# Kernel optimization log

Measured on AMD Instinct MI355X. Metric: run time of the kernel, lower is better.

The kernel has to match this reference:

```python
import jax, jax.numpy as jnp
import numpy as np

CELLS = 56
EPS = 1e-9

def setup_inputs() -> dict:
    key = jax.random.key(0)
    k1, k2 = jax.random.split(key)
    B = 512
    F = CELLS * CELLS * 15  # 47040 floats per sample
    output = jax.random.uniform(k1, (B, F), dtype=jnp.float32)
    target = jax.random.uniform(k2, (B, F), dtype=jnp.float32)
    return {"output": output, "target": target}

def reference(output, target):
    B = output.shape[0]
    # reshape flat vector into [B, cells^2, 15] slots: x,y,w,h,conf,classes[5:14]
    o = output.reshape(B, CELLS * CELLS, 15)
    t = target.reshape(B, CELLS * CELLS, 15)
    # coordinate loss: only x (slice [i*15 : i*15+1]) plus sqrt(w)/sqrt(h) terms
    coord = (o[..., 0] - t[..., 0]) ** 2 \
          + (jnp.sqrt(o[..., 2]) - jnp.sqrt(t[..., 2])) ** 2 \
          + (jnp.sqrt(o[..., 3]) - jnp.sqrt(t[..., 3])) ** 2
    # binary cross-entropy on confidence (slot 4)
    conf = -(t[..., 4] * jnp.log(o[..., 4] + EPS)
             + (1.0 - t[..., 4]) * jnp.log(1.0 - o[..., 4] + EPS))
    # class loss: sum of squared diffs over slots 5:14 (9 elements)
    cls = jnp.sum((t[..., 5:14] - o[..., 5:14]) ** 2, axis=-1)
    # cell is counted only if output x-coordinate is nonzero (torch.is_nonzero gate)
    mask = o[..., 0] != 0
    per_cell = jnp.where(mask, coord + conf + cls, 0.0)
    return jnp.sum(per_cell)
```

## Files before the change

### kernel.cpp

```cpp
#include <hip/hip_runtime.h>


constexpr int CPT = 256;
constexpr int TF  = CPT * 15;
#define EPSF 1e-9f

__global__ __launch_bounds__(256) void yolo_loss_kernel(
    const float* __restrict__ o, const float* __restrict__ t,
    float* __restrict__ out_sum, int n_cells)
{
    __shared__ __align__(16) float so[TF];
    __shared__ __align__(16) float st[TF];
    __shared__ float wsum[4];

    const int tid = threadIdx.x;
    const int n_tiles = (n_cells + CPT - 1) / CPT;
    const long lim4 = ((long)n_cells * 15) / 4;
    const float4* o4 = (const float4*)o;
    const float4* t4 = (const float4*)t;

    float acc = 0.f;

    for (int tile = blockIdx.x; tile < n_tiles; tile += gridDim.x) {
        __syncthreads();
        const long b4 = (long)tile * (TF / 4);
        #pragma unroll
        for (int i = tid; i < TF / 4; i += 256) {
            long g = b4 + i;
            if (g < lim4) {
                ((float4*)so)[i] = o4[g];
                ((float4*)st)[i] = t4[g];
            }
        }
        __syncthreads();

        const int cell = tile * CPT + tid;
        if (cell < n_cells) {
            const float* oc = so + tid * 15;
            const float* tc = st + tid * 15;
            const float o0 = oc[0];
            if (o0 != 0.f) {
                const float d0 = o0 - tc[0];
                const float dw = sqrtf(oc[2]) - sqrtf(tc[2]);
                const float dh = sqrtf(oc[3]) - sqrtf(tc[3]);
                const float tv = tc[4], ov = oc[4];
                const float conf = -(tv * __logf(ov + EPSF)
                                   + (1.f - tv) * __logf(1.f - ov + EPSF));
                float s = d0 * d0 + dw * dw + dh * dh + conf;
                #pragma unroll
                for (int k = 5; k < 14; ++k) {
                    const float d = tc[k] - oc[k];
                    s += d * d;
                }
                acc += s;
            }
        }
    }

    #pragma unroll
    for (int off = 32; off; off >>= 1) acc += __shfl_down(acc, off, 64);
    if ((tid & 63) == 0) wsum[tid >> 6] = acc;
    __syncthreads();
    if (tid == 0) atomicAdd(out_sum, wsum[0] + wsum[1] + wsum[2] + wsum[3]);
}

extern "C" void kernel_launch(void* const* d_in, const int* in_sizes, int n_in,
                              void* d_out, int out_size, void* d_ws, size_t ws_size,
                              hipStream_t stream) {
    const float* o = (const float*)d_in[0];
    const float* t = (const float*)d_in[1];
    float* out = (float*)d_out;
    const int n = in_sizes[0];
    const int n_cells = n / 15;

    hipMemsetAsync(out, 0, sizeof(float), stream);

    const int grid = 1024;
    yolo_loss_kernel<<<grid, 256, 0, stream>>>(o, t, out, n_cells);
}
```

Measured before the change: 207.4 us.

## Load four-cell groups directly into registers instead of staging through LDS

```diff
diff --git a/kernel.cpp b/kernel.cpp
--- a/kernel.cpp
+++ b/kernel.cpp
@@ -1,64 +1,79 @@
 #include <hip/hip_runtime.h>
 
 
-constexpr int CPT = 256;
-constexpr int TF  = CPT * 15;
 #define EPSF 1e-9f
 
 __global__ __launch_bounds__(256) void yolo_loss_kernel(
     const float* __restrict__ o, const float* __restrict__ t,
     float* __restrict__ out_sum, int n_cells)
 {
-    __shared__ __align__(16) float so[TF];
-    __shared__ __align__(16) float st[TF];
-    __shared__ float wsum[4];
-
     const int tid = threadIdx.x;
-    const int n_tiles = (n_cells + CPT - 1) / CPT;
-    const long lim4 = ((long)n_cells * 15) / 4;
-    const float4* o4 = (const float4*)o;
-    const float4* t4 = (const float4*)t;
+    const int g   = blockIdx.x * 256 + tid;
+    const int n_groups = n_cells >> 2;
 
     float acc = 0.f;
 
-    for (int tile = blockIdx.x; tile < n_tiles; tile += gridDim.x) {
-        __syncthreads();
-        const long b4 = (long)tile * (TF / 4);
+    if (g < n_groups) {
+        const float4* o4 = (const float4*)o + (size_t)g * 15;
+        const float4* t4 = (const float4*)t + (size_t)g * 15;
+
+        float4 ob[15], tb[15];
         #pragma unroll
-        for (int i = tid; i < TF / 4; i += 256) {
-            long g = b4 + i;
-            if (g < lim4) {
-                ((float4*)so)[i] = o4[g];
-                ((float4*)st)[i] = t4[g];
+        for (int j = 0; j < 15; ++j) { ob[j] = o4[j]; tb[j] = t4[j]; }
+        const float* os = (const float*)ob;
+        const float* ts = (const float*)tb;
+
+        float csum[4], x0[4];
+        #pragma unroll
+        for (int c = 0; c < 4; ++c) {
+            const float* oc = os + c * 15;
+            const float* tc = ts + c * 15;
+            x0[c] = oc[0];
+            const float d0 = oc[0] - tc[0];
+            const float dw = sqrtf(oc[2]) - sqrtf(tc[2]);
+            const float dh = sqrtf(oc[3]) - sqrtf(tc[3]);
+            const float tv = tc[4], ov = oc[4];
+            const float conf = -(tv * __logf(ov + EPSF)
+                               + (1.f - tv) * __logf(1.f - ov + EPSF));
+            float s = d0 * d0 + dw * dw + dh * dh + conf;
+            #pragma unroll
+            for (int k = 5; k < 14; ++k) {
+                const float d = tc[k] - oc[k];
+                s += d * d;
             }
+            csum[c] = s;
         }
-        __syncthreads();
+        #pragma unroll
+        for (int c = 0; c < 4; ++c)
+            acc += (x0[c] != 0.f) ? csum[c] : 0.f;
+    }
 
-        const int cell = tile * CPT + tid;
-        if (cell < n_cells) {
-            const float* oc = so + tid * 15;
-            const float* tc = st + tid * 15;
-            const float o0 = oc[0];
-            if (o0 != 0.f) {
-                const float d0 = o0 - tc[0];
-                const float dw = sqrtf(oc[2]) - sqrtf(tc[2]);
-                const float dh = sqrtf(oc[3]) - sqrtf(tc[3]);
-                const float tv = tc[4], ov = oc[4];
-                const float conf = -(tv * __logf(ov + EPSF)
-                                   + (1.f - tv) * __logf(1.f - ov + EPSF));
-                float s = d0 * d0 + dw * dw + dh * dh + conf;
-                #pragma unroll
-                for (int k = 5; k < 14; ++k) {
-                    const float d = tc[k] - oc[k];
-                    s += d * d;
-                }
-                acc += s;
+    const int tail_base = n_groups << 2;
+    const int n_tail = n_cells - tail_base;
+    if (blockIdx.x == 0 && tid < n_tail) {
+        const float* oc = o + (size_t)(tail_base + tid) * 15;
+        const float* tc = t + (size_t)(tail_base + tid) * 15;
+        const float o0 = oc[0];
+        if (o0 != 0.f) {
+            const float d0 = o0 - tc[0];
+            const float dw = sqrtf(oc[2]) - sqrtf(tc[2]);
+            const float dh = sqrtf(oc[3]) - sqrtf(tc[3]);
+            const float tv = tc[4], ov = oc[4];
+            const float conf = -(tv * __logf(ov + EPSF)
+                               + (1.f - tv) * __logf(1.f - ov + EPSF));
+            float s = d0 * d0 + dw * dw + dh * dh + conf;
+            #pragma unroll
+            for (int k = 5; k < 14; ++k) {
+                const float d = tc[k] - oc[k];
+                s += d * d;
             }
+            acc += s;
         }
     }
 
     #pragma unroll
     for (int off = 32; off; off >>= 1) acc += __shfl_down(acc, off, 64);
+    __shared__ float wsum[4];
     if ((tid & 63) == 0) wsum[tid >> 6] = acc;
     __syncthreads();
     if (tid == 0) atomicAdd(out_sum, wsum[0] + wsum[1] + wsum[2] + wsum[3]);
@@ -72,9 +87,10 @@
     float* out = (float*)d_out;
     const int n = in_sizes[0];
     const int n_cells = n / 15;
+    const int n_groups = n_cells >> 2;
+    const int grid = (n_groups + 255) / 256;
 
     hipMemsetAsync(out, 0, sizeof(float), stream);
 
-    const int grid = 1024;
     yolo_loss_kernel<<<grid, 256, 0, stream>>>(o, t, out, n_cells);
 }
```

Measured after the change: 250.8 us. +21.0%, slower.

## Process elements per float4 directly, dropping shared-memory cell staging

Applied to the files above, without the earlier changes.

```diff
diff --git a/kernel.cpp b/kernel.cpp
--- a/kernel.cpp
+++ b/kernel.cpp
@@ -1,64 +1,81 @@
 #include <hip/hip_runtime.h>
 
 
-constexpr int CPT = 256;
-constexpr int TF  = CPT * 15;
 #define EPSF 1e-9f
 
 __global__ __launch_bounds__(256) void yolo_loss_kernel(
     const float* __restrict__ o, const float* __restrict__ t,
-    float* __restrict__ out_sum, int n_cells)
+    float* __restrict__ out_sum, int n4, int n)
 {
-    __shared__ __align__(16) float so[TF];
-    __shared__ __align__(16) float st[TF];
-    __shared__ float wsum[4];
-
     const int tid = threadIdx.x;
-    const int n_tiles = (n_cells + CPT - 1) / CPT;
-    const long lim4 = ((long)n_cells * 15) / 4;
+    const int stride = gridDim.x * 256;
     const float4* o4 = (const float4*)o;
     const float4* t4 = (const float4*)t;
 
     float acc = 0.f;
 
-    for (int tile = blockIdx.x; tile < n_tiles; tile += gridDim.x) {
-        __syncthreads();
-        const long b4 = (long)tile * (TF / 4);
+    #pragma unroll 2
+    for (int i = blockIdx.x * 256 + tid; i < n4; i += stride) {
+        const float4 ov = o4[i];
+        const float4 tv = t4[i];
+
+        const unsigned e0    = (unsigned)i * 4u;
+        const unsigned cell0 = e0 / 15u;
+        const unsigned slot0 = e0 - cell0 * 15u;
+        const unsigned cell3 = (e0 + 3u) / 15u;
+        const float g_lo = o[(size_t)cell0 * 15u];
+        const float g_hi = o[(size_t)cell3 * 15u];
+
+        const float oe[4] = {ov.x, ov.y, ov.z, ov.w};
+        const float te[4] = {tv.x, tv.y, tv.z, tv.w};
+
         #pragma unroll
-        for (int i = tid; i < TF / 4; i += 256) {
-            long g = b4 + i;
-            if (g < lim4) {
-                ((float4*)so)[i] = o4[g];
-                ((float4*)st)[i] = t4[g];
-            }
+        for (int j = 0; j < 4; ++j) {
+            unsigned s = slot0 + (unsigned)j;
+            const bool wrap = s >= 15u;
+            s = wrap ? s - 15u : s;
+            const float gate = wrap ? g_hi : g_lo;
+            const float ox = oe[j], tx = te[j];
+
+            const bool issq = (s == 2u) | (s == 3u);
+            const float a = issq ? sqrtf(ox) : ox;
+            const float b = issq ? sqrtf(tx) : tx;
+            const float d = a - b;
+            const float sq = d * d;
+
+            const float bce = -(tx * __logf(ox + EPSF)
+                              + (1.f - tx) * __logf(1.f - ox + EPSF));
+
+            float c = (s == 4u) ? bce : sq;
+            c = (s == 1u || s == 14u) ? 0.f : c;
+            c = (gate != 0.f) ? c : 0.f;
+            acc += c;
         }
-        __syncthreads();
+    }
 
-        const int cell = tile * CPT + tid;
-        if (cell < n_cells) {
-            const float* oc = so + tid * 15;
-            const float* tc = st + tid * 15;
-            const float o0 = oc[0];
-            if (o0 != 0.f) {
-                const float d0 = o0 - tc[0];
-                const float dw = sqrtf(oc[2]) - sqrtf(tc[2]);
-                const float dh = sqrtf(oc[3]) - sqrtf(tc[3]);
-                const float tv = tc[4], ov = oc[4];
-                const float conf = -(tv * __logf(ov + EPSF)
-                                   + (1.f - tv) * __logf(1.f - ov + EPSF));
-                float s = d0 * d0 + dw * dw + dh * dh + conf;
-                #pragma unroll
-                for (int k = 5; k < 14; ++k) {
-                    const float d = tc[k] - oc[k];
-                    s += d * d;
-                }
-                acc += s;
-            }
-        }
+    const int tail0 = n4 * 4;
+    if (blockIdx.x == 0 && tid < n - tail0) {
+        const unsigned e = (unsigned)(tail0 + tid);
+        const unsigned cell = e / 15u;
+        const unsigned s = e - cell * 15u;
+        const float gate = o[(size_t)cell * 15u];
+        const float ox = o[e], tx = t[e];
+        const bool issq = (s == 2u) | (s == 3u);
+        const float a = issq ? sqrtf(ox) : ox;
+        const float b = issq ? sqrtf(tx) : tx;
+        const float d = a - b;
+        const float sq = d * d;
+        const float bce = -(tx * __logf(ox + EPSF)
+                          + (1.f - tx) * __logf(1.f - ox + EPSF));
+        float c = (s == 4u) ? bce : sq;
+        c = (s == 1u || s == 14u) ? 0.f : c;
+        c = (gate != 0.f) ? c : 0.f;
+        acc += c;
     }
 
     #pragma unroll
     for (int off = 32; off; off >>= 1) acc += __shfl_down(acc, off, 64);
+    __shared__ float wsum[4];
     if ((tid & 63) == 0) wsum[tid >> 6] = acc;
     __syncthreads();
     if (tid == 0) atomicAdd(out_sum, wsum[0] + wsum[1] + wsum[2] + wsum[3]);
@@ -71,10 +88,10 @@
     const float* t = (const float*)d_in[1];
     float* out = (float*)d_out;
     const int n = in_sizes[0];
-    const int n_cells = n / 15;
+    const int n4 = n / 4;
 
     hipMemsetAsync(out, 0, sizeof(float), stream);
 
-    const int grid = 1024;
-    yolo_loss_kernel<<<grid, 256, 0, stream>>>(o, t, out, n_cells);
+    const int grid = 2048;
+    yolo_loss_kernel<<<grid, 256, 0, stream>>>(o, t, out, n4, n);
 }
```

Result: slower. 216.8 us (+4.6%).

## Stage tiles via direct global-to-LDS loads in single-wave blocks

Applied to the files above, without the earlier changes.

```diff
diff --git a/kernel.cpp b/kernel.cpp
--- a/kernel.cpp
+++ b/kernel.cpp
@@ -1,67 +1,70 @@
 #include <hip/hip_runtime.h>
 
 
-constexpr int CPT = 256;
-constexpr int TF  = CPT * 15;
 #define EPSF 1e-9f
 
-__global__ __launch_bounds__(256) void yolo_loss_kernel(
+typedef __attribute__((address_space(3))) void lds_void_t;
+typedef const __attribute__((address_space(1))) void gmem_void_t;
+
+__device__ __forceinline__ void gload_lds4(const float* g, float* l) {
+    __builtin_amdgcn_global_load_lds((gmem_void_t*)g, (lds_void_t*)l, 4, 0, 0);
+}
+
+__device__ __forceinline__ float cell_loss(const float* __restrict__ oc,
+                                           const float* __restrict__ tc) {
+    const float o0 = oc[0];
+    const float d0 = o0 - tc[0];
+    const float ow = oc[2], tw = tc[2], oh = oc[3], th = tc[3];
+    const float w2 = ow + tw - 2.f * sqrtf(ow * tw);
+    const float h2 = oh + th - 2.f * sqrtf(oh * th);
+    const float ov = oc[4], tv = tc[4];
+    const float conf = -(tv * __logf(ov + EPSF)
+                       + (1.f - tv) * __logf(1.f - ov + EPSF));
+    float s = d0 * d0 + w2 + h2 + conf;
+    #pragma unroll
+    for (int k = 5; k < 14; ++k) { const float d = tc[k] - oc[k]; s += d * d; }
+    return (o0 != 0.f) ? s : 0.f;
+}
+
+__global__ __launch_bounds__(64) void yolo_loss_kernel(
     const float* __restrict__ o, const float* __restrict__ t,
     float* __restrict__ out_sum, int n_cells)
 {
-    __shared__ __align__(16) float so[TF];
-    __shared__ __align__(16) float st[TF];
-    __shared__ float wsum[4];
+    __shared__ float so[960];
+    __shared__ float st[960];
 
-    const int tid = threadIdx.x;
-    const int n_tiles = (n_cells + CPT - 1) / CPT;
-    const long lim4 = ((long)n_cells * 15) / 4;
-    const float4* o4 = (const float4*)o;
-    const float4* t4 = (const float4*)t;
+    const int lane = threadIdx.x;
+    const int n_tiles = n_cells >> 6;
 
     float acc = 0.f;
 
     for (int tile = blockIdx.x; tile < n_tiles; tile += gridDim.x) {
-        __syncthreads();
-        const long b4 = (long)tile * (TF / 4);
-        #pragma unroll
-        for (int i = tid; i < TF / 4; i += 256) {
-            long g = b4 + i;
-            if (g < lim4) {
-                ((float4*)so)[i] = o4[g];
-                ((float4*)st)[i] = t4[g];
-            }
-        }
+        __builtin_amdgcn_s_waitcnt(0xC07F);
         __syncthreads();
 
-        const int cell = tile * CPT + tid;
-        if (cell < n_cells) {
-            const float* oc = so + tid * 15;
-            const float* tc = st + tid * 15;
-            const float o0 = oc[0];
-            if (o0 != 0.f) {
-                const float d0 = o0 - tc[0];
-                const float dw = sqrtf(oc[2]) - sqrtf(tc[2]);
-                const float dh = sqrtf(oc[3]) - sqrtf(tc[3]);
-                const float tv = tc[4], ov = oc[4];
-                const float conf = -(tv * __logf(ov + EPSF)
-                                   + (1.f - tv) * __logf(1.f - ov + EPSF));
-                float s = d0 * d0 + dw * dw + dh * dh + conf;
-                #pragma unroll
-                for (int k = 5; k < 14; ++k) {
-                    const float d = tc[k] - oc[k];
-                    s += d * d;
-                }
-                acc += s;
-            }
-        }
+        const size_t base = (size_t)tile * 960;
+        const float* go = o + base + lane;
+        const float* gt = t + base + lane;
+        #pragma unroll
+        for (int k = 0; k < 15; ++k) gload_lds4(go + k * 64, &so[k * 64]);
+        #pragma unroll
+        for (int k = 0; k < 15; ++k) gload_lds4(gt + k * 64, &st[k * 64]);
+
+        __builtin_amdgcn_s_waitcnt(0x0F70);
+        __syncthreads();
+
+        acc += cell_loss(so + lane * 15, st + lane * 15);
+    }
+
+    const int tail0 = n_tiles << 6;
+    if (blockIdx.x == 0 && lane < (n_cells - tail0)) {
+        const size_t c = (size_t)(tail0 + lane) * 15;
+        acc += cell_loss(o + c, t + c);
     }
 
     #pragma unroll
     for (int off = 32; off; off >>= 1) acc += __shfl_down(acc, off, 64);
-    if ((tid & 63) == 0) wsum[tid >> 6] = acc;
-    __syncthreads();
-    if (tid == 0) atomicAdd(out_sum, wsum[0] + wsum[1] + wsum[2] + wsum[3]);
+    if (lane == 0) atomicAdd(out_sum, acc);
 }
 
 extern "C" void kernel_launch(void* const* d_in, const int* in_sizes, int n_in,
@@ -75,6 +78,6 @@
 
     hipMemsetAsync(out, 0, sizeof(float), stream);
 
-    const int grid = 1024;
-    yolo_loss_kernel<<<grid, 256, 0, stream>>>(o, t, out, n_cells);
+    const int grid = 4096;
+    yolo_loss_kernel<<<grid, 64, 0, stream>>>(o, t, out, n_cells);
 }
```

Measured after the change: 231.7 us. 11.7% more time.
